# Kernel optimization log

Measured on AMD Instinct MI355X. Metric: run time of the kernel, lower is better.

The kernel has to match this reference:

```python
import jax, jax.numpy as jnp
import numpy as np

N_HEADS = 16
EMBD = 1024
D_HEAD = EMBD // N_HEADS

def setup_inputs() -> dict:
    key = jax.random.key(0)
    ks = jax.random.split(key, 5)
    x = jax.random.normal(ks[0], (2, 2048, EMBD), dtype=jnp.float32)
    # Linear weights stored torch-style [out, in]; apply as x @ W.T + b
    W_in = jax.random.normal(ks[1], (3 * EMBD, EMBD), dtype=jnp.float32) * (EMBD ** -0.5)
    b_in = jax.random.normal(ks[2], (3 * EMBD,), dtype=jnp.float32) * 0.01
    W_out = jax.random.normal(ks[3], (EMBD, EMBD), dtype=jnp.float32) * (EMBD ** -0.5)
    b_out = jax.random.normal(ks[4], (EMBD,), dtype=jnp.float32) * 0.01
    return {"x": x, "W_in": W_in, "b_in": b_in, "W_out": W_out, "b_out": b_out}

def reference(x, W_in, b_in, W_out, b_out):
    B, S, D = x.shape
    qkv = x @ W_in.T + b_in                      # [B, S, 3D]
    q, k, v = jnp.split(qkv, 3, axis=-1)
    def heads(t):
        return t.reshape(B, S, N_HEADS, D_HEAD).transpose(0, 2, 1, 3)  # [B,H,S,d]
    q, k, v = heads(q), heads(k), heads(v)
    scale = 1.0 / jnp.sqrt(jnp.float32(D_HEAD))
    scores = jnp.einsum('bhqd,bhkd->bhqk', q, k) * scale
    weights = jax.nn.softmax(scores, axis=-1)
    out = jnp.einsum('bhqk,bhkd->bhqd', weights, v)  # [B,H,S,d]
    out = out.transpose(0, 2, 1, 3).reshape(B, S, D)
    return out @ W_out.T + b_out
```

## Files before the change

kernel.cpp:

```cpp
#include <hip/hip_runtime.h>
#include <cstdint>

#define EMBD 1024
#define NH 16
#define DH 64
#define BB 2
#define SS 2048
#define M_TOT (BB*SS)
#define N_QKV (3*EMBD)

typedef __bf16 bf16_t;
typedef bf16_t bf16x8 __attribute__((ext_vector_type(8)));
typedef float f32x4 __attribute__((ext_vector_type(4)));
typedef unsigned short u16;
typedef unsigned int u32;

static __device__ __forceinline__ u16 f2bf(float f) {
    union { float f; unsigned u; } c; c.f = f;
    unsigned u = c.u;
    unsigned r = (u + 0x7FFFu + ((u >> 16) & 1u)) >> 16;
    return (u16)r;
}

#define GLDS16(gp, lp) \
    __builtin_amdgcn_global_load_lds((const __attribute__((address_space(1))) void*)(gp), \
                                     (__attribute__((address_space(3))) void*)(lp), 16, 0, 0)

#define NX8 (M_TOT * EMBD / 8)
#define NWI8 (N_QKV * EMBD / 8)
#define NWO8 (EMBD * EMBD / 8)
__global__ void cast_all(const float* __restrict__ x, const float* __restrict__ wi,
                         const float* __restrict__ wo, u16* __restrict__ xb,
                         u16* __restrict__ wib, u16* __restrict__ wob) {
    int i = blockIdx.x * blockDim.x + threadIdx.x;
    const float* s; u16* d; int off;
    if (i < NX8)              { s = x;  d = xb;  off = i; }
    else if (i < NX8 + NWI8)  { s = wi; d = wib; off = i - NX8; }
    else                      { s = wo; d = wob; off = i - NX8 - NWI8; }
    const float4* s4 = (const float4*)s;
    float4 a = s4[2 * off];
    float4 b = s4[2 * off + 1];
    union { u16 u[8]; uint4 v; } r;
    r.u[0] = f2bf(a.x); r.u[1] = f2bf(a.y); r.u[2] = f2bf(a.z); r.u[3] = f2bf(a.w);
    r.u[4] = f2bf(b.x); r.u[5] = f2bf(b.y); r.u[6] = f2bf(b.z); r.u[7] = f2bf(b.w);
    ((uint4*)d)[off] = r.v;
}

#define QSCALE (0.125f * 1.4426950408889634f)
__global__ __launch_bounds__(256) void gemm_qkv(
    const u16* __restrict__ Xb,
    const u16* __restrict__ Wb,
    const float* __restrict__ b_in,
    u16* __restrict__ Q, u16* __restrict__ Kf, u16* __restrict__ Vpf)
{
    __shared__ u16 As[128 * 32];
    __shared__ u16 Bs[128 * 32];
    const int t = threadIdx.x;
    const int lane = t & 63;
    const int wave = t >> 6;
    const int wm = wave >> 1, wn = wave & 1;
    const int quad = lane >> 4, l16 = lane & 15;
    const int m0 = blockIdx.y * 128, n0 = blockIdx.x * 128;

    const int s0i = t, s1i = 256 + t;
    const u16* ga0 = Xb + (size_t)(m0 + (s0i >> 2)) * EMBD + (s0i & 3) * 8;
    const u16* ga1 = Xb + (size_t)(m0 + (s1i >> 2)) * EMBD + (s1i & 3) * 8;
    const u16* gb0 = Wb + (size_t)(n0 + (s0i >> 2)) * EMBD + (s0i & 3) * 8;
    const u16* gb1 = Wb + (size_t)(n0 + (s1i >> 2)) * EMBD + (s1i & 3) * 8;
    u16* lA0 = As + s0i * 8; u16* lA1 = As + s1i * 8;
    u16* lB0 = Bs + s0i * 8; u16* lB1 = Bs + s1i * 8;

    f32x4 acc[4][4] = {};

    for (int k0 = 0; k0 < EMBD; k0 += 32) {
        GLDS16(ga0 + k0, lA0); GLDS16(ga1 + k0, lA1);
        GLDS16(gb0 + k0, lB0); GLDS16(gb1 + k0, lB1);
        __syncthreads();
        bf16x8 af[4], bfr[4];
#pragma unroll
        for (int im = 0; im < 4; ++im)
            af[im] = *(const bf16x8*)(As + (wm * 64 + im * 16 + l16) * 32 + quad * 8);
#pragma unroll
        for (int in = 0; in < 4; ++in)
            bfr[in] = *(const bf16x8*)(Bs + (wn * 64 + in * 16 + l16) * 32 + quad * 8);
#pragma unroll
        for (int im = 0; im < 4; ++im)
#pragma unroll
            for (int in = 0; in < 4; ++in)
                acc[im][in] = __builtin_amdgcn_mfma_f32_16x16x32_bf16(
                    af[im], bfr[in], acc[im][in], 0, 0, 0);
        __syncthreads();
    }

#pragma unroll
    for (int im = 0; im < 4; ++im) {
        int rbase = m0 + wm * 64 + im * 16 + quad * 4;
        int b = rbase >> 11, ss = rbase & (SS - 1);
#pragma unroll
        for (int in = 0; in < 4; ++in) {
            int col = n0 + wn * 64 + in * 16 + l16;
            float bias = b_in[col];
            float v0 = acc[im][in][0] + bias;
            float v1 = acc[im][in][1] + bias;
            float v2 = acc[im][in][2] + bias;
            float v3 = acc[im][in][3] + bias;
            if (col < EMBD) {
                int h = col >> 6, d = col & 63;
                u16* qp = Q + (((size_t)(b * NH + h) * SS) + ss) * DH + d;
                qp[0]      = f2bf(v0 * QSCALE);
                qp[DH]     = f2bf(v1 * QSCALE);
                qp[2 * DH] = f2bf(v2 * QSCALE);
                qp[3 * DH] = f2bf(v3 * QSCALE);
            } else if (col < 2 * EMBD) {
                int c = col - EMBD; int h = c >> 6, d = c & 63;
                u16* kp = Kf + (size_t)(b * NH + h) * SS * DH
                          + (ss >> 4) * 1024 + (d >> 5) * 512
                          + (ss & 15) * 32 + ((d >> 3) & 3) * 8 + (d & 7);
                kp[0]  = f2bf(v0);
                kp[32] = f2bf(v1);
                kp[64] = f2bf(v2);
                kp[96] = f2bf(v3);
            } else {
                int c = col - 2 * EMBD; int h = c >> 6, d = c & 63;
                int p32 = ((ss >> 2) & 3) * 8 + ((ss >> 4) & 1) * 4;
                u32 lo = (u32)f2bf(v0) | ((u32)f2bf(v1) << 16);
                u32 hi = (u32)f2bf(v2) | ((u32)f2bf(v3) << 16);
                uint2 pk; pk.x = lo; pk.y = hi;
                *(uint2*)(Vpf + (size_t)(b * NH + h) * SS * DH
                          + (ss >> 5) * 2048 + (d >> 4) * 512 + (d & 15) * 32 + p32) = pk;
            }
        }
    }
}

#define OST 72
__global__ __launch_bounds__(256, 2) void attn(
    const u16* __restrict__ Q, const u16* __restrict__ Kf,
    const u16* __restrict__ Vpf, u16* __restrict__ AO)
{
    __shared__ u16 KV[2][8192];
    const int t = threadIdx.x;
    const int lane = t & 63, w = t >> 6;
    const int quad = lane >> 4, l16 = lane & 15;
    const int b0 = blockIdx.x;
    const int bh = (b0 & 7) * 4 + ((b0 >> 3) & 3);
    const int qt = b0 >> 5;
    const int q0 = qt * 128 + w * 32;

    const u16* Qh = Q + ((size_t)bh * SS + q0) * DH;
    const u16* Kh = Kf + (size_t)bh * SS * DH;
    const u16* Vh = Vpf + (size_t)bh * SS * DH;

    bf16x8 qb[2][2];
#pragma unroll
    for (int qi = 0; qi < 2; ++qi) {
        qb[qi][0] = *(const bf16x8*)(Qh + (qi * 16 + l16) * DH + quad * 8);
        qb[qi][1] = *(const bf16x8*)(Qh + (qi * 16 + l16) * DH + 32 + quad * 8);
    }

    f32x4 o[2][4] = {};
    float lsum[2] = {0.f, 0.f};

    GLDS16(Kh + t * 8,        &KV[0][0] + t * 8);
    GLDS16(Kh + 2048 + t * 8, &KV[0][0] + 2048 + t * 8);
    GLDS16(Vh + t * 8,        &KV[0][4096] + t * 8);
    GLDS16(Vh + 2048 + t * 8, &KV[0][4096] + 2048 + t * 8);

    for (int it = 0; it < SS / 64; ++it) {
        asm volatile("s_waitcnt vmcnt(0)" ::: "memory");
        __syncthreads();
        if (it + 1 < SS / 64) {
            const u16* kc = Kh + (it + 1) * 4096;
            const u16* vc = Vh + (it + 1) * 4096;
            u16* kb = &KV[(it + 1) & 1][0];
            u16* vb = &KV[(it + 1) & 1][4096];
            GLDS16(kc + t * 8,        kb + t * 8);
            GLDS16(kc + 2048 + t * 8, kb + 2048 + t * 8);
            GLDS16(vc + t * 8,        vb + t * 8);
            GLDS16(vc + 2048 + t * 8, vb + 2048 + t * 8);
        }
        const u16* Kb = &KV[it & 1][0];
        const u16* Vb = &KV[it & 1][4096];
#pragma unroll
        for (int g = 0; g < 2; ++g) {
            bf16x8 ka00 = *(const bf16x8*)(Kb + (2 * g) * 1024 +       l16 * 32 + quad * 8);
            bf16x8 ka01 = *(const bf16x8*)(Kb + (2 * g) * 1024 + 512 + l16 * 32 + quad * 8);
            bf16x8 ka10 = *(const bf16x8*)(Kb + (2 * g + 1) * 1024 +       l16 * 32 + quad * 8);
            bf16x8 ka11 = *(const bf16x8*)(Kb + (2 * g + 1) * 1024 + 512 + l16 * 32 + quad * 8);
            bf16x8 va0 = *(const bf16x8*)(Vb + g * 2048 +        l16 * 32 + quad * 8);
            bf16x8 va1 = *(const bf16x8*)(Vb + g * 2048 + 512  + l16 * 32 + quad * 8);
            bf16x8 va2 = *(const bf16x8*)(Vb + g * 2048 + 1024 + l16 * 32 + quad * 8);
            bf16x8 va3 = *(const bf16x8*)(Vb + g * 2048 + 1536 + l16 * 32 + quad * 8);
            bf16x8 pb[2];
#pragma unroll
            for (int qi = 0; qi < 2; ++qi) {
                f32x4 z0 = {0.f, 0.f, 0.f, 0.f};
                f32x4 z1 = {0.f, 0.f, 0.f, 0.f};
                z0 = __builtin_amdgcn_mfma_f32_16x16x32_bf16(ka00, qb[qi][0], z0, 0, 0, 0);
                z0 = __builtin_amdgcn_mfma_f32_16x16x32_bf16(ka01, qb[qi][1], z0, 0, 0, 0);
                z1 = __builtin_amdgcn_mfma_f32_16x16x32_bf16(ka10, qb[qi][0], z1, 0, 0, 0);
                z1 = __builtin_amdgcn_mfma_f32_16x16x32_bf16(ka11, qb[qi][1], z1, 0, 0, 0);
                u32 ue[8];
                float ls = 0.f;
#pragma unroll
                for (int j = 0; j < 4; ++j) {
                    float e0 = __builtin_amdgcn_exp2f(z0[j]);
                    float e1 = __builtin_amdgcn_exp2f(z1[j]);
                    ls += e0 + e1;
                    union { float f; u32 v; } c0, c1;
                    c0.f = e0; c1.f = e1;
                    ue[j] = c0.v + 0x8000u;
                    ue[4 + j] = c1.v + 0x8000u;
                }
                lsum[qi] += ls;
                union { uint4 u; bf16x8 b; } cv;
                cv.u.x = __builtin_amdgcn_perm(ue[1], ue[0], 0x07060302u);
                cv.u.y = __builtin_amdgcn_perm(ue[3], ue[2], 0x07060302u);
                cv.u.z = __builtin_amdgcn_perm(ue[5], ue[4], 0x07060302u);
                cv.u.w = __builtin_amdgcn_perm(ue[7], ue[6], 0x07060302u);
                pb[qi] = cv.b;
            }
            o[0][0] = __builtin_amdgcn_mfma_f32_16x16x32_bf16(va0, pb[0], o[0][0], 0, 0, 0);
            o[0][1] = __builtin_amdgcn_mfma_f32_16x16x32_bf16(va1, pb[0], o[0][1], 0, 0, 0);
            o[0][2] = __builtin_amdgcn_mfma_f32_16x16x32_bf16(va2, pb[0], o[0][2], 0, 0, 0);
            o[0][3] = __builtin_amdgcn_mfma_f32_16x16x32_bf16(va3, pb[0], o[0][3], 0, 0, 0);
            o[1][0] = __builtin_amdgcn_mfma_f32_16x16x32_bf16(va0, pb[1], o[1][0], 0, 0, 0);
            o[1][1] = __builtin_amdgcn_mfma_f32_16x16x32_bf16(va1, pb[1], o[1][1], 0, 0, 0);
            o[1][2] = __builtin_amdgcn_mfma_f32_16x16x32_bf16(va2, pb[1], o[1][2], 0, 0, 0);
            o[1][3] = __builtin_amdgcn_mfma_f32_16x16x32_bf16(va3, pb[1], o[1][3], 0, 0, 0);
        }
    }

    float rl[2];
#pragma unroll
    for (int qi = 0; qi < 2; ++qi) {
        float v = lsum[qi];
        v += __shfl_xor(v, 16, 64);
        v += __shfl_xor(v, 32, 64);
        rl[qi] = 1.0f / v;
    }
    __syncthreads();
    u16* Ksc = &KV[0][0];
#pragma unroll
    for (int qi = 0; qi < 2; ++qi)
#pragma unroll
        for (int dt = 0; dt < 4; ++dt)
#pragma unroll
            for (int jj = 0; jj < 2; ++jj) {
                u32 lo_ = (u32)f2bf(o[qi][dt][2 * jj] * rl[qi]);
                u32 hi_ = (u32)f2bf(o[qi][dt][2 * jj + 1] * rl[qi]);
                *(u32*)(Ksc + (w * 32 + qi * 16 + l16) * OST + dt * 16 + quad * 4 + jj * 2) =
                    lo_ | (hi_ << 16);
            }
    __syncthreads();
    const int b = bh >> 4, h = bh & 15;
#pragma unroll
    for (int i = 0; i < 4; ++i) {
        int idx = i * 256 + t;
        int q = idx >> 3, c = idx & 7;
        uint4 vv = *(const uint4*)(Ksc + q * OST + c * 8);
        *(uint4*)(AO + ((size_t)(b * SS + qt * 128 + q)) * EMBD + h * DH + c * 8) = vv;
    }
}

__global__ __launch_bounds__(256) void gemm_out(
    const u16* __restrict__ Ab,
    const u16* __restrict__ Wb,
    const float* __restrict__ b_out,
    float* __restrict__ Out)
{
    __shared__ u16 As[128 * 32];
    __shared__ u16 Bs[128 * 32];
    const int t = threadIdx.x;
    const int lane = t & 63;
    const int wave = t >> 6;
    const int wm = wave >> 1, wn = wave & 1;
    const int quad = lane >> 4, l16 = lane & 15;
    const int m0 = blockIdx.y * 128, n0 = blockIdx.x * 128;

    const int s0i = t, s1i = 256 + t;
    const u16* ga0 = Ab + (size_t)(m0 + (s0i >> 2)) * EMBD + (s0i & 3) * 8;
    const u16* ga1 = Ab + (size_t)(m0 + (s1i >> 2)) * EMBD + (s1i & 3) * 8;
    const u16* gb0 = Wb + (size_t)(n0 + (s0i >> 2)) * EMBD + (s0i & 3) * 8;
    const u16* gb1 = Wb + (size_t)(n0 + (s1i >> 2)) * EMBD + (s1i & 3) * 8;
    u16* lA0 = As + s0i * 8; u16* lA1 = As + s1i * 8;
    u16* lB0 = Bs + s0i * 8; u16* lB1 = Bs + s1i * 8;

    f32x4 acc[4][4] = {};

    for (int k0 = 0; k0 < EMBD; k0 += 32) {
        GLDS16(ga0 + k0, lA0); GLDS16(ga1 + k0, lA1);
        GLDS16(gb0 + k0, lB0); GLDS16(gb1 + k0, lB1);
        __syncthreads();
        bf16x8 af[4], bfr[4];
#pragma unroll
        for (int im = 0; im < 4; ++im)
            af[im] = *(const bf16x8*)(As + (wm * 64 + im * 16 + l16) * 32 + quad * 8);
#pragma unroll
        for (int in = 0; in < 4; ++in)
            bfr[in] = *(const bf16x8*)(Bs + (wn * 64 + in * 16 + l16) * 32 + quad * 8);
#pragma unroll
        for (int im = 0; im < 4; ++im)
#pragma unroll
            for (int in = 0; in < 4; ++in)
                acc[im][in] = __builtin_amdgcn_mfma_f32_16x16x32_bf16(
                    af[im], bfr[in], acc[im][in], 0, 0, 0);
        __syncthreads();
    }

#pragma unroll
    for (int im = 0; im < 4; ++im) {
        int rbase = m0 + wm * 64 + im * 16 + quad * 4;
#pragma unroll
        for (int in = 0; in < 4; ++in) {
            int col = n0 + wn * 64 + in * 16 + l16;
            float bias = b_out[col];
#pragma unroll
            for (int j = 0; j < 4; ++j)
                Out[(size_t)(rbase + j) * EMBD + col] = acc[im][in][j] + bias;
        }
    }
}

extern "C" void kernel_launch(void* const* d_in, const int* in_sizes, int n_in,
                              void* d_out, int out_size, void* d_ws, size_t ws_size,
                              hipStream_t stream)
{
    (void)in_sizes; (void)n_in; (void)out_size; (void)ws_size;
    const float* x     = (const float*)d_in[0];
    const float* W_in  = (const float*)d_in[1];
    const float* b_in  = (const float*)d_in[2];
    const float* W_out = (const float*)d_in[3];
    const float* b_out = (const float*)d_in[4];
    float* out = (float*)d_out;

    char* ws = (char*)d_ws;
    u16* xb  = (u16*)(ws);
    u16* wib = (u16*)(ws + 8u  * 1024 * 1024);
    u16* wob = (u16*)(ws + 14u * 1024 * 1024);
    u16* Qw  = (u16*)(ws + 16u * 1024 * 1024);
    u16* Kw  = (u16*)(ws + 24u * 1024 * 1024);
    u16* Vpw = (u16*)(ws + 32u * 1024 * 1024);
    u16* AO  = (u16*)(ws + 40u * 1024 * 1024);

    cast_all<<<(NX8 + NWI8 + NWO8) / 256, 256, 0, stream>>>(x, W_in, W_out, xb, wib, wob);
    gemm_qkv<<<dim3(N_QKV / 128, M_TOT / 128), 256, 0, stream>>>(xb, wib, b_in, Qw, Kw, Vpw);
    attn<<<512, 256, 0, stream>>>(Qw, Kw, Vpw, AO);
    gemm_out<<<dim3(EMBD / 128, M_TOT / 128), 256, 0, stream>>>(AO, wob, b_out, out);
}
```

Baseline: 180.8 us.

## Double-buffer LDS tiles in QKV and output GEMMs to overlap loads with MFMA

Both projection GEMMs now keep two LDS stage buffers. The global-to-LDS copy of the next K-slice is issued right after the barrier, while MFMAs run on the current slice, and one of the two barriers per iteration is dropped. The goal is to hide global load latency behind compute instead of serializing load, sync and compute. The cost is doubled LDS per block, which may reduce occupancy. Correctness relies on the single barrier ordering the reads of the previous buffer before it is overwritten.

```diff
diff --git a/kernel.cpp b/kernel.cpp
--- a/kernel.cpp
+++ b/kernel.cpp
@@ -53,8 +53,7 @@
     const float* __restrict__ b_in,
     u16* __restrict__ Q, u16* __restrict__ Kf, u16* __restrict__ Vpf)
 {
-    __shared__ u16 As[128 * 32];
-    __shared__ u16 Bs[128 * 32];
+    __shared__ u16 AB[2][8192];
     const int t = threadIdx.x;
     const int lane = t & 63;
     const int wave = t >> 6;
@@ -67,15 +66,30 @@
     const u16* ga1 = Xb + (size_t)(m0 + (s1i >> 2)) * EMBD + (s1i & 3) * 8;
     const u16* gb0 = Wb + (size_t)(n0 + (s0i >> 2)) * EMBD + (s0i & 3) * 8;
     const u16* gb1 = Wb + (size_t)(n0 + (s1i >> 2)) * EMBD + (s1i & 3) * 8;
-    u16* lA0 = As + s0i * 8; u16* lA1 = As + s1i * 8;
-    u16* lB0 = Bs + s0i * 8; u16* lB1 = Bs + s1i * 8;
 
     f32x4 acc[4][4] = {};
 
-    for (int k0 = 0; k0 < EMBD; k0 += 32) {
-        GLDS16(ga0 + k0, lA0); GLDS16(ga1 + k0, lA1);
-        GLDS16(gb0 + k0, lB0); GLDS16(gb1 + k0, lB1);
+    {
+        u16* buf = &AB[0][0];
+        GLDS16(ga0, buf + s0i * 8);
+        GLDS16(ga1, buf + s1i * 8);
+        GLDS16(gb0, buf + 4096 + s0i * 8);
+        GLDS16(gb1, buf + 4096 + s1i * 8);
+    }
+
+    for (int it = 0; it < EMBD / 32; ++it) {
+        asm volatile("s_waitcnt vmcnt(0)" ::: "memory");
         __syncthreads();
+        if (it + 1 < EMBD / 32) {
+            int k0 = (it + 1) * 32;
+            u16* buf = &AB[(it + 1) & 1][0];
+            GLDS16(ga0 + k0, buf + s0i * 8);
+            GLDS16(ga1 + k0, buf + s1i * 8);
+            GLDS16(gb0 + k0, buf + 4096 + s0i * 8);
+            GLDS16(gb1 + k0, buf + 4096 + s1i * 8);
+        }
+        const u16* As = &AB[it & 1][0];
+        const u16* Bs = &AB[it & 1][4096];
         bf16x8 af[4], bfr[4];
 #pragma unroll
         for (int im = 0; im < 4; ++im)
@@ -89,7 +103,6 @@
             for (int in = 0; in < 4; ++in)
                 acc[im][in] = __builtin_amdgcn_mfma_f32_16x16x32_bf16(
                     af[im], bfr[in], acc[im][in], 0, 0, 0);
-        __syncthreads();
     }
 
 #pragma unroll
@@ -269,8 +282,7 @@
     const float* __restrict__ b_out,
     float* __restrict__ Out)
 {
-    __shared__ u16 As[128 * 32];
-    __shared__ u16 Bs[128 * 32];
+    __shared__ u16 AB[2][8192];
     const int t = threadIdx.x;
     const int lane = t & 63;
     const int wave = t >> 6;
@@ -283,15 +295,30 @@
     const u16* ga1 = Ab + (size_t)(m0 + (s1i >> 2)) * EMBD + (s1i & 3) * 8;
     const u16* gb0 = Wb + (size_t)(n0 + (s0i >> 2)) * EMBD + (s0i & 3) * 8;
     const u16* gb1 = Wb + (size_t)(n0 + (s1i >> 2)) * EMBD + (s1i & 3) * 8;
-    u16* lA0 = As + s0i * 8; u16* lA1 = As + s1i * 8;
-    u16* lB0 = Bs + s0i * 8; u16* lB1 = Bs + s1i * 8;
 
     f32x4 acc[4][4] = {};
 
-    for (int k0 = 0; k0 < EMBD; k0 += 32) {
-        GLDS16(ga0 + k0, lA0); GLDS16(ga1 + k0, lA1);
-        GLDS16(gb0 + k0, lB0); GLDS16(gb1 + k0, lB1);
+    {
+        u16* buf = &AB[0][0];
+        GLDS16(ga0, buf + s0i * 8);
+        GLDS16(ga1, buf + s1i * 8);
+        GLDS16(gb0, buf + 4096 + s0i * 8);
+        GLDS16(gb1, buf + 4096 + s1i * 8);
+    }
+
+    for (int it = 0; it < EMBD / 32; ++it) {
+        asm volatile("s_waitcnt vmcnt(0)" ::: "memory");
         __syncthreads();
+        if (it + 1 < EMBD / 32) {
+            int k0 = (it + 1) * 32;
+            u16* buf = &AB[(it + 1) & 1][0];
+            GLDS16(ga0 + k0, buf + s0i * 8);
+            GLDS16(ga1 + k0, buf + s1i * 8);
+            GLDS16(gb0 + k0, buf + 4096 + s0i * 8);
+            GLDS16(gb1 + k0, buf + 4096 + s1i * 8);
+        }
+        const u16* As = &AB[it & 1][0];
+        const u16* Bs = &AB[it & 1][4096];
         bf16x8 af[4], bfr[4];
 #pragma unroll
         for (int im = 0; im < 4; ++im)
@@ -305,7 +332,6 @@
             for (int in = 0; in < 4; ++in)
                 acc[im][in] = __builtin_amdgcn_mfma_f32_16x16x32_bf16(
                     af[im], bfr[in], acc[im][in], 0, 0, 0);
-        __syncthreads();
     }
 
 #pragma unroll
```

New measurement: 180.9 us. About the same (+0.0%).
